# Optimization experiments

Measured on AMD Instinct MI355X. Metric: run time of the kernel, lower is better.

The kernel has to match this reference:

```python
import jax, jax.numpy as jnp
import numpy as np

N = 50000   # nodes
E = 800000  # edges (avg degree 16)
G = 256     # graphs in batch
IN = 64; H = 128; K = 8; C = 10; L = 3
TAU = 1.0


def _bn(x, g, b, eps=1e-5):
    # BatchNorm1d training-mode forward: batch stats over the row dim.
    m = x.mean(0)
    v = x.var(0)
    return (x - m) * jax.lax.rsqrt(v + eps) * g + b


def _ln(x, g, b, eps=1e-5):
    m = x.mean(-1, keepdims=True)
    v = x.var(-1, keepdims=True)
    return (x - m) * jax.lax.rsqrt(v + eps) * g + b


def setup_inputs() -> dict:
    key = jax.random.key(0)
    ks = jax.random.split(key, 16)
    p = lambda k, shape: jax.random.normal(k, shape, jnp.float32) * 0.05
    u = jax.random.uniform(ks[2], (N, K), minval=1e-10, maxval=1.0)
    return {
        "x": jax.random.normal(ks[0], (N, IN), jnp.float32),
        "edge_index": jax.random.randint(ks[1], (2, E), 0, N, dtype=jnp.int32),
        "batch": (jnp.arange(N, dtype=jnp.int32) * G) // N,  # sorted, all graphs present
        "gumbel": -jnp.log(-jnp.log(u)),  # fixed Gumbel(0,1) noise
        "inp_w": p(ks[3], (IN, H)), "inp_b": jnp.zeros(H),
        "elin_w": p(ks[4], (L, 1, H)), "elin_b": jnp.zeros((L, H)),
        "mlp1_w": p(ks[5], (L, H, H)), "mlp1_b": jnp.zeros((L, H)),
        "mlpbn_g": jnp.ones((L, H)), "mlpbn_b": jnp.zeros((L, H)),
        "mlp2_w": p(ks[6], (L, H, H)), "mlp2_b": jnp.zeros((L, H)),
        "bn_g": jnp.ones((L, H)), "bn_b": jnp.zeros((L, H)),
        "bh1_w": p(ks[7], (H, H // 2)), "bh1_b": jnp.zeros(H // 2),
        "bh2_w": p(ks[8], (H // 2, K)), "bh2_b": jnp.zeros(K),
        "bm_w": p(ks[9], (H, H)), "bm_b": jnp.zeros(H),
        "ln_g": jnp.ones(H), "ln_b": jnp.zeros(H),
        "clf1_w": p(ks[10], (2 * H, H)), "clf1_b": jnp.zeros(H),
        "clfbn_g": jnp.ones(H), "clfbn_b": jnp.zeros(H),
        "clf2_w": p(ks[11], (H, C)), "clf2_b": jnp.zeros(C),
    }


def reference(x, edge_index, batch, gumbel, inp_w, inp_b, elin_w, elin_b,
              mlp1_w, mlp1_b, mlpbn_g, mlpbn_b, mlp2_w, mlp2_b, bn_g, bn_b,
              bh1_w, bh1_b, bh2_w, bh2_b, bm_w, bm_b, ln_g, ln_b,
              clf1_w, clf1_b, clfbn_g, clfbn_b, clf2_w, clf2_b):
    src, dst = edge_index[0], edge_index[1]
    h = x @ inp_w + inp_b  # [N,H]
    for l in range(L):  # GINEConv stack (eps=0, dummy edge attr = ones[E,1])
        e_emb = elin_w[l][0] + elin_b[l]          # ones @ W + b -> single [H] vector
        msg = jax.nn.relu(h[src] + e_emb)          # gather + add, [E,H]
        aggr = jax.ops.segment_sum(msg, dst, num_segments=N)  # scatter-add
        z = h + aggr                               # (1+eps)*x + aggr, eps=0
        z = jax.nn.relu(_bn(z @ mlp1_w[l] + mlp1_b[l], mlpbn_g[l], mlpbn_b[l]))
        z = z @ mlp2_w[l] + mlp2_b[l]
        h = jax.nn.relu(_bn(z, bn_g[l], bn_b[l]))
    # blob assignment via gumbel-softmax (soft)
    logits = jax.nn.relu(h @ bh1_w + bh1_b) @ bh2_w + bh2_b  # [N,K]
    assign = jax.nn.softmax((logits + gumbel) / TAU, axis=-1)
    counts = jax.ops.segment_sum(jnp.ones((N,), h.dtype), batch, num_segments=G)
    gmean = jax.ops.segment_sum(h, batch, num_segments=G) / counts[:, None]  # [G,H]
    # per-graph weighted blob pooling, vectorized over graphs via segment_sum
    num = jax.ops.segment_sum(assign[:, :, None] * h[:, None, :], batch, num_segments=G)  # [G,K,H]
    den = jax.ops.segment_sum(assign, batch, num_segments=G)  # [G,K]
    blobs = num / (den[:, :, None] + 1e-8)
    blobs = _ln(jax.nn.relu(blobs @ bm_w + bm_b), ln_g, ln_b)
    blob_emb = blobs.max(axis=1)  # [G,H]
    z = jnp.concatenate([gmean, blob_emb], axis=-1)  # [G,2H]
    z = jax.nn.relu(_bn(z @ clf1_w + clf1_b, clfbn_g, clfbn_b))
    return z @ clf2_w + clf2_b  # [G,C]
```

## Files before the change

### kernel.cpp

```cpp
#include <hip/hip_runtime.h>
#include <hip/hip_bf16.h>


#define HH 128
typedef unsigned short u16;
typedef unsigned int u32;
typedef __attribute__((ext_vector_type(8))) short bf16x8;
typedef __attribute__((ext_vector_type(4))) float f32x4;

__device__ __forceinline__ void atomAddF(float* p, float v) { unsafeAtomicAdd(p, v); }

__device__ __forceinline__ u16 f2bf(float f) {
    u32 u = __float_as_uint(f);
    u += 0x7fffu + ((u >> 16) & 1u);
    return (u16)(u >> 16);
}
__device__ __forceinline__ float bf2f_lo(u32 u) { return __uint_as_float(u << 16); }
__device__ __forceinline__ float bf2f_hi(u32 u) { return __uint_as_float(u & 0xffff0000u); }
__device__ __forceinline__ void split2(float v, u16& hi, u16& lo) {
    u16 h_ = f2bf(v);
    float hf = __uint_as_float(((u32)h_) << 16);
    hi = h_;
    lo = f2bf(v - hf);
}
__device__ __forceinline__ u32 swz(u32 row, u32 kByte, u32 strideB) {
    return (row * strideB + kByte) ^ ((row & 7u) << 4);
}

#define WTOT (8192 + 6 * 16384)

__global__ void k_prep(const float* __restrict__ inp_w, const float* __restrict__ m1,
                       const float* __restrict__ m2, u16* __restrict__ Whi,
                       u16* __restrict__ Wlo) {
    int b = blockIdx.x;
    int t = threadIdx.x;
    if (b == 0) {
        for (int idx = t; idx < 128 * 64; idx += 256) {
            int c = idx >> 6, k = idx & 63;
            u16 hi, lo;
            split2(inp_w[k * 128 + c], hi, lo);
            Whi[idx] = hi; Wlo[idx] = lo;
        }
    } else {
        const float* W = (b <= 3) ? m1 + (size_t)(b - 1) * 16384
                                  : m2 + (size_t)(b - 4) * 16384;
        u16* dh = Whi + 8192 + (size_t)(b - 1) * 16384;
        u16* dl = Wlo + 8192 + (size_t)(b - 1) * 16384;
        for (int idx = t; idx < 16384; idx += 256) {
            int c = idx >> 7, k = idx & 127;
            u16 hi, lo;
            split2(W[k * 128 + c], hi, lo);
            dh[idx] = hi; dl[idx] = lo;
        }
    }
}

__global__ void k_hist(const int* __restrict__ ei, int* __restrict__ deg, int E) {
    int i4 = blockIdx.x * 256 + threadIdx.x;
    int e0 = i4 * 4;
    if (e0 + 3 < E) {
        int4 d = *(const int4*)(ei + E + e0);
        atomicAdd(&deg[d.x], 1);
        atomicAdd(&deg[d.y], 1);
        atomicAdd(&deg[d.z], 1);
        atomicAdd(&deg[d.w], 1);
    } else {
        for (int e = e0; e < E; e++) atomicAdd(&deg[ei[E + e]], 1);
    }
}

__global__ void k_bsum(const int* __restrict__ deg, int* __restrict__ bsum, int N) {
    int t = threadIdx.x;
    int i = blockIdx.x * 256 + t;
    int v = (i < N) ? deg[i] : 0;
    for (int o = 32; o; o >>= 1) v += __shfl_down(v, o);
    __shared__ int ws_[4];
    if ((t & 63) == 0) ws_[t >> 6] = v;
    __syncthreads();
    if (t == 0) bsum[blockIdx.x] = ws_[0] + ws_[1] + ws_[2] + ws_[3];
}

__global__ void k_scan1(const int* __restrict__ bsum, int* __restrict__ boff,
                        int* __restrict__ rowptrN, int nch) {
    int t = threadIdx.x;
    int v = (t < nch) ? bsum[t] : 0;
    int l = t & 63, w = t >> 6;
    int sv = v;
    for (int o = 1; o < 64; o <<= 1) { int u = __shfl_up(sv, o); if (l >= o) sv += u; }
    __shared__ int wsum[4];
    if (l == 63) wsum[w] = sv;
    __syncthreads();
    int add = 0;
    for (int j = 0; j < w; j++) add += wsum[j];
    if (t < nch) boff[t] = sv - v + add;
    if (t == nch - 1) *rowptrN = sv + add;
}

__global__ void k_scan2(const int* __restrict__ deg, const int* __restrict__ boff,
                        int* __restrict__ rowptr, int* __restrict__ cursor, int N) {
    int b = blockIdx.x, t = threadIdx.x, i = b * 256 + t;
    int v = (i < N) ? deg[i] : 0;
    int l = t & 63, w = t >> 6;
    int sv = v;
    for (int o = 1; o < 64; o <<= 1) { int u = __shfl_up(sv, o); if (l >= o) sv += u; }
    __shared__ int wsum[4];
    if (l == 63) wsum[w] = sv;
    __syncthreads();
    int add = boff[b];
    for (int j = 0; j < w; j++) add += wsum[j];
    if (i < N) { int e = sv - v + add; rowptr[i] = e; cursor[i] = e; }
}

__global__ void k_fill(const int* __restrict__ ei, int* __restrict__ cursor,
                       int* __restrict__ col, int E) {
    int i4 = blockIdx.x * 256 + threadIdx.x;
    int e0 = i4 * 4;
    if (e0 + 3 < E) {
        int4 s = *(const int4*)(ei + e0);
        int4 d = *(const int4*)(ei + E + e0);
        int p0 = atomicAdd(&cursor[d.x], 1);
        int p1 = atomicAdd(&cursor[d.y], 1);
        int p2 = atomicAdd(&cursor[d.z], 1);
        int p3 = atomicAdd(&cursor[d.w], 1);
        col[p0] = s.x;
        col[p1] = s.y;
        col[p2] = s.z;
        col[p3] = s.w;
    } else {
        for (int e = e0; e < E; e++) {
            int pos = atomicAdd(&cursor[ei[E + e]], 1);
            col[pos] = ei[e];
        }
    }
}

template <int KD, int MODE, bool STATS, bool FOUT, bool BOUT>
__global__ __launch_bounds__(512) void k_mgemm(
    const float* __restrict__ inf, const u16* __restrict__ inhi,
    const u16* __restrict__ inlo, const u16* __restrict__ Whi,
    const u16* __restrict__ Wlo, const float* __restrict__ bias,
    const float* __restrict__ statsIn, const float* __restrict__ gamma,
    const float* __restrict__ beta, float invN,
    float* __restrict__ out, u16* __restrict__ outb,
    float* __restrict__ statsOut, int Nrows, int ntiles) {
    __shared__ u16 s_Bhi[128 * KD];
    __shared__ u16 s_Blo[128 * KD];
    __shared__ float s_red[2][8][128];
    __shared__ float s_sc[128], s_sh[128];
    const int t = threadIdx.x;
    constexpr u32 STR = KD * 2;
    constexpr int KCB = KD / 8;
    constexpr int NB = (128 * KCB) / 512;
    constexpr int NF = KD / 32;

#pragma unroll
    for (int i = 0; i < NB; i++) {
        int idx = i * 512 + t;
        int c = idx / KCB, kc = idx % KCB;
        u32 off = swz(c, kc * 16, STR);
        *(uint4*)((char*)s_Bhi + off) = *(const uint4*)(Whi + (size_t)c * KD + kc * 8);
        *(uint4*)((char*)s_Blo + off) = *(const uint4*)(Wlo + (size_t)c * KD + kc * 8);
    }
    if (MODE == 1 && t < 128) {
        float m = statsIn[t] * invN;
        float var = statsIn[128 + t] * invN - m * m;
        float s = gamma[t] * rsqrtf(var + 1e-5f);
        s_sc[t] = s;
        s_sh[t] = beta[t] - m * s;
    }
    __syncthreads();

    const int l = t & 63, w = t >> 6;
    const int c0 = l & 15;
    const int ksub = (l >> 4) * 8;
    const u32 kOffB = (u32)(l >> 4) * 16u;

    for (int tile = blockIdx.x; tile < ntiles; tile += gridDim.x) {
        const int row = tile * 128 + w * 16 + c0;
        const bool rv = row < Nrows;

        bf16x8 ah[NF], al[NF];
        if (MODE == 2) {
#pragma unroll
            for (int kk = 0; kk < NF; kk++) {
                int k0 = kk * 32 + ksub;
                if (rv) {
                    ah[kk] = *(const bf16x8*)(inhi + (size_t)row * KD + k0);
                    al[kk] = *(const bf16x8*)(inlo + (size_t)row * KD + k0);
                } else {
                    uint4 z = {0, 0, 0, 0};
                    ah[kk] = *(bf16x8*)&z;
                    al[kk] = *(bf16x8*)&z;
                }
            }
        } else {
#pragma unroll
            for (int kk = 0; kk < NF; kk++) {
                int k0 = kk * 32 + ksub;
                float4 v0 = {0.f, 0.f, 0.f, 0.f}, v1 = {0.f, 0.f, 0.f, 0.f};
                if (rv) {
                    v0 = *(const float4*)(inf + (size_t)row * KD + k0);
                    v1 = *(const float4*)(inf + (size_t)row * KD + k0 + 4);
                }
                float vv[8] = {v0.x, v0.y, v0.z, v0.w, v1.x, v1.y, v1.z, v1.w};
                uint4 uh, ul;
                u32* ph = (u32*)&uh;
                u32* pl = (u32*)&ul;
#pragma unroll
                for (int p = 0; p < 4; p++) {
                    float a0 = vv[2 * p], a1 = vv[2 * p + 1];
                    if (MODE == 1) {
                        a0 = fmaxf(a0 * s_sc[k0 + 2 * p] + s_sh[k0 + 2 * p], 0.f);
                        a1 = fmaxf(a1 * s_sc[k0 + 2 * p + 1] + s_sh[k0 + 2 * p + 1], 0.f);
                    }
                    u16 h0, l0, h1, l1;
                    split2(a0, h0, l0);
                    split2(a1, h1, l1);
                    ph[p] = (u32)h0 | ((u32)h1 << 16);
                    pl[p] = (u32)l0 | ((u32)l1 << 16);
                }
                ah[kk] = *(bf16x8*)&uh;
                al[kk] = *(bf16x8*)&ul;
            }
        }

        f32x4 acc[8];
#pragma unroll
        for (int n = 0; n < 8; n++) acc[n] = (f32x4){0.f, 0.f, 0.f, 0.f};
#pragma unroll
        for (int kk = 0; kk < NF; kk++) {
            u32 kb = kk * 64 + kOffB;
#pragma unroll
            for (int n = 0; n < 8; n++) {
                u32 ob = swz(n * 16 + c0, kb, STR);
                bf16x8 bh = *(const bf16x8*)((char*)s_Bhi + ob);
                bf16x8 bl = *(const bf16x8*)((char*)s_Blo + ob);
                acc[n] = __builtin_amdgcn_mfma_f32_16x16x32_bf16(ah[kk], bh, acc[n], 0, 0, 0);
                acc[n] = __builtin_amdgcn_mfma_f32_16x16x32_bf16(al[kk], bh, acc[n], 0, 0, 0);
                acc[n] = __builtin_amdgcn_mfma_f32_16x16x32_bf16(ah[kk], bl, acc[n], 0, 0, 0);
            }
        }

        const int rbase = tile * 128 + w * 16 + ((l >> 4) << 2);
#pragma unroll
        for (int n = 0; n < 8; n++) {
            const int colc = n * 16 + c0;
            const float bv = bias[colc];
            float s = 0.f, q = 0.f;
#pragma unroll
            for (int j = 0; j < 4; j++) {
                int gr = rbase + j;
                if (gr < Nrows) {
                    float v = acc[n][j] + bv;
                    if (FOUT) out[(size_t)gr * HH + colc] = v;
                    if (BOUT) outb[(size_t)gr * HH + colc] = f2bf(v);
                    s += v;
                    q += v * v;
                }
            }
            if (STATS) {
                s += __shfl_xor(s, 16); s += __shfl_xor(s, 32);
                q += __shfl_xor(q, 16); q += __shfl_xor(q, 32);
                if (l < 16) {
                    s_red[0][w][n * 16 + l] = s;
                    s_red[1][w][n * 16 + l] = q;
                }
            }
        }
        if (STATS) {
            __syncthreads();
            if (t < 128) {
                float S = 0.f, Q = 0.f;
#pragma unroll
                for (int ww = 0; ww < 8; ww++) { S += s_red[0][ww][t]; Q += s_red[1][ww][t]; }
                atomAddF(&statsOut[t], S);
                atomAddF(&statsOut[HH + t], Q);
            }
            __syncthreads();
        }
    }
}

__global__ __launch_bounds__(256) void k_gather(
    const u16* __restrict__ hb,
    const int* __restrict__ rowptr, const int* __restrict__ col,
    const float* __restrict__ ew, const float* __restrict__ eb,
    u16* __restrict__ zhi, u16* __restrict__ zlo, int N) {
    __shared__ float2 s_part[2][64];
    const int wv = threadIdx.x >> 6;
    const int lane = threadIdx.x & 63;
    const int node = blockIdx.x * 2 + (wv >> 1);
    const int hf = wv & 1;
    const int c2 = lane * 2;
    float2 acc = {0.f, 0.f};
    const bool valid = node < N;
    float2 ee = {0.f, 0.f};
    if (valid) {
        ee.x = ew[c2] + eb[c2];
        ee.y = ew[c2 + 1] + eb[c2 + 1];
        const int s = rowptr[node], eend = rowptr[node + 1];
        int e = s + hf;
        for (; e + 14 < eend; e += 16) {
            int s0 = col[e], s1 = col[e + 2], s2 = col[e + 4], s3 = col[e + 6];
            int s4 = col[e + 8], s5 = col[e + 10], s6 = col[e + 12], s7 = col[e + 14];
            u32 u0 = *(const u32*)(hb + (size_t)s0 * HH + c2);
            u32 u1 = *(const u32*)(hb + (size_t)s1 * HH + c2);
            u32 u2 = *(const u32*)(hb + (size_t)s2 * HH + c2);
            u32 u3 = *(const u32*)(hb + (size_t)s3 * HH + c2);
            u32 u4 = *(const u32*)(hb + (size_t)s4 * HH + c2);
            u32 u5 = *(const u32*)(hb + (size_t)s5 * HH + c2);
            u32 u6 = *(const u32*)(hb + (size_t)s6 * HH + c2);
            u32 u7 = *(const u32*)(hb + (size_t)s7 * HH + c2);
            acc.x += fmaxf(bf2f_lo(u0) + ee.x, 0.f) + fmaxf(bf2f_lo(u1) + ee.x, 0.f) +
                     fmaxf(bf2f_lo(u2) + ee.x, 0.f) + fmaxf(bf2f_lo(u3) + ee.x, 0.f) +
                     fmaxf(bf2f_lo(u4) + ee.x, 0.f) + fmaxf(bf2f_lo(u5) + ee.x, 0.f) +
                     fmaxf(bf2f_lo(u6) + ee.x, 0.f) + fmaxf(bf2f_lo(u7) + ee.x, 0.f);
            acc.y += fmaxf(bf2f_hi(u0) + ee.y, 0.f) + fmaxf(bf2f_hi(u1) + ee.y, 0.f) +
                     fmaxf(bf2f_hi(u2) + ee.y, 0.f) + fmaxf(bf2f_hi(u3) + ee.y, 0.f) +
                     fmaxf(bf2f_hi(u4) + ee.y, 0.f) + fmaxf(bf2f_hi(u5) + ee.y, 0.f) +
                     fmaxf(bf2f_hi(u6) + ee.y, 0.f) + fmaxf(bf2f_hi(u7) + ee.y, 0.f);
        }
        for (; e + 6 < eend; e += 8) {
            int s0 = col[e], s1 = col[e + 2], s2 = col[e + 4], s3 = col[e + 6];
            u32 u0 = *(const u32*)(hb + (size_t)s0 * HH + c2);
            u32 u1 = *(const u32*)(hb + (size_t)s1 * HH + c2);
            u32 u2 = *(const u32*)(hb + (size_t)s2 * HH + c2);
            u32 u3 = *(const u32*)(hb + (size_t)s3 * HH + c2);
            acc.x += fmaxf(bf2f_lo(u0) + ee.x, 0.f) + fmaxf(bf2f_lo(u1) + ee.x, 0.f) +
                     fmaxf(bf2f_lo(u2) + ee.x, 0.f) + fmaxf(bf2f_lo(u3) + ee.x, 0.f);
            acc.y += fmaxf(bf2f_hi(u0) + ee.y, 0.f) + fmaxf(bf2f_hi(u1) + ee.y, 0.f) +
                     fmaxf(bf2f_hi(u2) + ee.y, 0.f) + fmaxf(bf2f_hi(u3) + ee.y, 0.f);
        }
        for (; e < eend; e += 2) {
            u32 u0 = *(const u32*)(hb + (size_t)col[e] * HH + c2);
            acc.x += fmaxf(bf2f_lo(u0) + ee.x, 0.f);
            acc.y += fmaxf(bf2f_hi(u0) + ee.y, 0.f);
        }
    }
    if (hf) s_part[wv >> 1][lane] = acc;
    __syncthreads();
    if (!hf && valid) {
        float2 p = s_part[wv >> 1][lane];
        u32 un = *(const u32*)(hb + (size_t)node * HH + c2);
        float zx = bf2f_lo(un) + acc.x + p.x;
        float zy = bf2f_hi(un) + acc.y + p.y;
        u16 h0, h1, l0, l1;
        split2(zx, h0, l0);
        split2(zy, h1, l1);
        *(u32*)(zhi + (size_t)node * HH + c2) = (u32)h0 | ((u32)h1 << 16);
        *(u32*)(zlo + (size_t)node * HH + c2) = (u32)l0 | ((u32)l1 << 16);
    }
}

template <bool WF>
__global__ void k_bnrelu(const float* __restrict__ t, const float* __restrict__ stats,
                         const float* __restrict__ g, const float* __restrict__ b,
                         float invN, float* __restrict__ h, u16* __restrict__ hb,
                         int total4) {
    int i = blockIdx.x * 256 + threadIdx.x;
    if (i >= total4) return;
    int c4 = (i & 31) << 2;
    float sc[4], sh[4];
#pragma unroll
    for (int j = 0; j < 4; j++) {
        float m = stats[c4 + j] * invN;
        float var = stats[128 + c4 + j] * invN - m * m;
        float s = g[c4 + j] * rsqrtf(var + 1e-5f);
        sc[j] = s;
        sh[j] = b[c4 + j] - m * s;
    }
    float4 v = *(const float4*)(t + (size_t)i * 4);
    float4 o;
    o.x = fmaxf(v.x * sc[0] + sh[0], 0.f);
    o.y = fmaxf(v.y * sc[1] + sh[1], 0.f);
    o.z = fmaxf(v.z * sc[2] + sh[2], 0.f);
    o.w = fmaxf(v.w * sc[3] + sh[3], 0.f);
    if (WF) *(float4*)(h + (size_t)i * 4) = o;
    uint2 p = {(u32)f2bf(o.x) | ((u32)f2bf(o.y) << 16),
               (u32)f2bf(o.z) | ((u32)f2bf(o.w) << 16)};
    *(uint2*)(hb + (size_t)i * 4) = p;
}

__global__ __launch_bounds__(256) void k_assign(
    const float* __restrict__ h, const float* __restrict__ gum,
    const float* __restrict__ w1, const float* __restrict__ b1,
    const float* __restrict__ w2, const float* __restrict__ b2,
    float* __restrict__ assign, int N) {
    __shared__ float s_w1[128 * 64];
    __shared__ float s_w2[64 * 8];
    __shared__ float s_h[32][128];
    __shared__ float s_hid[32][64];
    const int t = threadIdx.x;
    const int n0 = blockIdx.x * 32;
    for (int i = t; i < 128 * 64; i += 256) s_w1[i] = w1[i];
    for (int i = t; i < 512; i += 256) s_w2[i] = w2[i];
    for (int i = t; i < 32 * 32; i += 256) {
        int r = i >> 5, c4 = (i & 31) << 2;
        int gn = n0 + r;
        float4 v = {0.f, 0.f, 0.f, 0.f};
        if (gn < N) v = *(const float4*)(h + (size_t)gn * HH + c4);
        *(float4*)(&s_h[r][c4]) = v;
    }
    __syncthreads();
    for (int o = t; o < 32 * 64; o += 256) {
        int nn = o >> 6, j = o & 63;
        float acc = b1[j];
        for (int k = 0; k < 128; k++) acc = fmaf(s_h[nn][k], s_w1[k * 64 + j], acc);
        s_hid[nn][j] = fmaxf(acc, 0.f);
    }
    __syncthreads();
    int nn = t >> 3, kk = t & 7;
    int gn = n0 + nn;
    float a = b2[kk];
    for (int j = 0; j < 64; j++) a = fmaf(s_hid[nn][j], s_w2[j * 8 + kk], a);
    if (gn < N) a += gum[(size_t)gn * 8 + kk];
    float m = a;
    m = fmaxf(m, __shfl_xor(m, 1));
    m = fmaxf(m, __shfl_xor(m, 2));
    m = fmaxf(m, __shfl_xor(m, 4));
    float e = expf(a - m);
    float s = e;
    s += __shfl_xor(s, 1); s += __shfl_xor(s, 2); s += __shfl_xor(s, 4);
    if (gn < N) assign[(size_t)gn * 8 + kk] = e / s;
}

__device__ __forceinline__ int lowerb(const int* __restrict__ arr, int n, int val) {
    int lo = 0, hi = n;
    while (lo < hi) {
        int mid = (lo + hi) >> 1;
        if (arr[mid] < val) lo = mid + 1;
        else hi = mid;
    }
    return lo;
}

__global__ __launch_bounds__(1024) void k_pool(
    const float* __restrict__ h, const float* __restrict__ assign,
    const int* __restrict__ batch, float* __restrict__ gmean,
    float* __restrict__ num, float* __restrict__ den, int N) {
    __shared__ float4 s_num[4][8][32];
    __shared__ float4 s_gm[4][32];
    __shared__ float s_den[4][8];
    const int g = blockIdx.x;
    const int t = threadIdx.x;
    const int ns = t >> 8;
    const int k = (t >> 5) & 7;
    const int lane = t & 31;
    const int c4 = lane << 2;
    const int start = lowerb(batch, N, g);
    const int end = lowerb(batch, N, g + 1);
    float4 an = {0.f, 0.f, 0.f, 0.f};
    float4 gm = {0.f, 0.f, 0.f, 0.f};
    float ad = 0.f;
    for (int n = start + ns; n < end; n += 4) {
        float a = assign[(size_t)n * 8 + k];
        const float4 hv = *(const float4*)(h + (size_t)n * HH + c4);
        an.x = fmaf(a, hv.x, an.x);
        an.y = fmaf(a, hv.y, an.y);
        an.z = fmaf(a, hv.z, an.z);
        an.w = fmaf(a, hv.w, an.w);
        if (k == 0) { gm.x += hv.x; gm.y += hv.y; gm.z += hv.z; gm.w += hv.w; }
        ad += a;
    }
    s_num[ns][k][lane] = an;
    if (k == 0) s_gm[ns][lane] = gm;
    if (lane == 0) s_den[ns][k] = ad;
    __syncthreads();
    if (t < 256) {
        float4 a0 = s_num[0][k][lane], a1 = s_num[1][k][lane];
        float4 a2 = s_num[2][k][lane], a3 = s_num[3][k][lane];
        float4 o = {a0.x + a1.x + a2.x + a3.x, a0.y + a1.y + a2.y + a3.y,
                    a0.z + a1.z + a2.z + a3.z, a0.w + a1.w + a2.w + a3.w};
        *(float4*)(num + ((size_t)g * 8 + k) * HH + c4) = o;
        if (t < 32) {
            float4 g0 = s_gm[0][lane], g1 = s_gm[1][lane];
            float4 g2 = s_gm[2][lane], g3 = s_gm[3][lane];
            int cnt = end - start;
            float inv = 1.f / (float)(cnt > 0 ? cnt : 1);
            float4 om = {(g0.x + g1.x + g2.x + g3.x) * inv,
                         (g0.y + g1.y + g2.y + g3.y) * inv,
                         (g0.z + g1.z + g2.z + g3.z) * inv,
                         (g0.w + g1.w + g2.w + g3.w) * inv};
            *(float4*)(gmean + (size_t)g * HH + c4) = om;
        }
        if (t < 8) den[(size_t)g * 8 + t] =
            s_den[0][t] + s_den[1][t] + s_den[2][t] + s_den[3][t];
    }
}

__global__ void k_blob(const float* __restrict__ num, const float* __restrict__ den,
                       const float* __restrict__ w, const float* __restrict__ b,
                       const float* __restrict__ lg, const float* __restrict__ lb,
                       float* __restrict__ blobs) {
    const int gk = blockIdx.x;
    const int c = threadIdx.x;
    __shared__ float srow[128];
    __shared__ float red[4];
    float d = den[gk] + 1e-8f;
    srow[c] = num[(size_t)gk * HH + c] / d;
    __syncthreads();
    float acc = b[c];
    for (int j = 0; j < 128; j++) acc = fmaf(srow[j], w[j * HH + c], acc);
    float y = fmaxf(acc, 0.f);
    float s = y, q = y * y;
    for (int off = 32; off > 0; off >>= 1) {
        s += __shfl_down(s, off);
        q += __shfl_down(q, off);
    }
    if ((c & 63) == 0) { red[(c >> 6) * 2] = s; red[(c >> 6) * 2 + 1] = q; }
    __syncthreads();
    float S = red[0] + red[2], Q = red[1] + red[3];
    float m = S * (1.f / 128.f);
    float var = Q * (1.f / 128.f) - m * m;
    blobs[(size_t)gk * HH + c] = (y - m) * rsqrtf(var + 1e-5f) * lg[c] + lb[c];
}

__global__ void k_clf1(const float* __restrict__ gmean, const float* __restrict__ blobs,
                       const float* __restrict__ w, const float* __restrict__ bias,
                       float* __restrict__ t4, float* __restrict__ stats) {
    int g = blockIdx.x;
    int c = threadIdx.x;
    __shared__ float s[256];
    float m = blobs[((size_t)g * 8) * HH + c];
#pragma unroll
    for (int k = 1; k < 8; k++) m = fmaxf(m, blobs[((size_t)g * 8 + k) * HH + c]);
    s[c] = gmean[(size_t)g * HH + c];
    s[128 + c] = m;
    __syncthreads();
    float acc = bias[c];
    for (int j = 0; j < 256; j++) acc = fmaf(s[j], w[j * HH + c], acc);
    t4[(size_t)g * HH + c] = acc;
    atomAddF(&stats[c], acc);
    atomAddF(&stats[HH + c], acc * acc);
}

__global__ void k_clf2(const float* __restrict__ t4, const float* __restrict__ stats,
                       const float* __restrict__ g_, const float* __restrict__ b_,
                       float invG, const float* __restrict__ w,
                       const float* __restrict__ bias, float* __restrict__ out) {
    int g = blockIdx.x;
    int t = threadIdx.x;
    __shared__ float s[128];
    float m = stats[t] * invG;
    float var = stats[128 + t] * invG - m * m;
    float sc = g_[t] * rsqrtf(var + 1e-5f);
    float sh = b_[t] - m * sc;
    s[t] = fmaxf(t4[(size_t)g * HH + t] * sc + sh, 0.f);
    __syncthreads();
    if (t < 10) {
        float acc = bias[t];
        for (int j = 0; j < 128; j++) acc = fmaf(s[j], w[j * 10 + t], acc);
        out[(size_t)g * 10 + t] = acc;
    }
}

extern "C" void kernel_launch(void* const* d_in, const int* in_sizes, int n_in,
                              void* d_out, int out_size, void* d_ws, size_t ws_size,
                              hipStream_t stream) {
    const float* x      = (const float*)d_in[0];
    const int*   ei     = (const int*)d_in[1];
    const int*   batch  = (const int*)d_in[2];
    const float* gumbel = (const float*)d_in[3];
    const float* inp_w  = (const float*)d_in[4];
    const float* inp_b  = (const float*)d_in[5];
    const float* elin_w = (const float*)d_in[6];
    const float* elin_b = (const float*)d_in[7];
    const float* mlp1_w = (const float*)d_in[8];
    const float* mlp1_b = (const float*)d_in[9];
    const float* mlpbn_g = (const float*)d_in[10];
    const float* mlpbn_b = (const float*)d_in[11];
    const float* mlp2_w = (const float*)d_in[12];
    const float* mlp2_b = (const float*)d_in[13];
    const float* bn_g   = (const float*)d_in[14];
    const float* bn_b   = (const float*)d_in[15];
    const float* bh1_w  = (const float*)d_in[16];
    const float* bh1_b  = (const float*)d_in[17];
    const float* bh2_w  = (const float*)d_in[18];
    const float* bh2_b  = (const float*)d_in[19];
    const float* bm_w   = (const float*)d_in[20];
    const float* bm_b   = (const float*)d_in[21];
    const float* ln_g   = (const float*)d_in[22];
    const float* ln_b   = (const float*)d_in[23];
    const float* clf1_w = (const float*)d_in[24];
    const float* clf1_b = (const float*)d_in[25];
    const float* clfbn_g = (const float*)d_in[26];
    const float* clfbn_b = (const float*)d_in[27];
    const float* clf2_w = (const float*)d_in[28];
    const float* clf2_b = (const float*)d_in[29];
    float* out = (float*)d_out;

    const int N = in_sizes[0] / 64;
    const int E = in_sizes[1] / 2;
    const int G = out_size / 10;

    float* ws = (float*)d_ws;
    float* h      = ws;
    float* zbuf   = h + (size_t)N * HH;
    float* t1     = zbuf + (size_t)N * HH;
    float* assign = t1 + (size_t)N * HH;
    float* gmean  = assign + (size_t)N * 8;
    float* num    = gmean + (size_t)G * HH;
    float* den    = num + (size_t)G * 8 * HH;
    float* blobs  = den + (size_t)G * 8;
    float* t4     = blobs + (size_t)G * 8 * HH;
    float* statsA = t4 + (size_t)G * HH;
    u16* Whi = (u16*)(statsA + 7 * 256);
    u16* Wlo = Whi + WTOT;
    int* rowptr = (int*)(Wlo + WTOT);
    int* cursor = rowptr + (N + 1);
    int* colidx = cursor + N;
    int* bsum   = colidx + E;
    int* boff   = bsum + 256;
    u16* hb  = (u16*)t1;
    u16* zhi = (u16*)zbuf;
    u16* zlo = zhi + (size_t)N * HH;
    float* t2 = zbuf;

    const dim3 B256(256), B128(128), B512(512), B1024(1024);
    const int ntiles = (N + 127) / 128;
    const int gg = ntiles < 512 ? ntiles : 512;
    const int nch = (N + 255) / 256;
    const int e4 = (E + 4 * 256 - 1) / (4 * 256);
    const float invN = 1.f / (float)N;
    const float invG = 1.f / (float)G;

    k_prep<<<7, B256, 0, stream>>>(inp_w, mlp1_w, mlp2_w, Whi, Wlo);
    hipMemsetAsync(cursor, 0, (size_t)N * sizeof(int), stream);
    hipMemsetAsync(statsA, 0, 7 * 256 * sizeof(float), stream);
    k_hist<<<e4, B256, 0, stream>>>(ei, cursor, E);
    k_bsum<<<nch, B256, 0, stream>>>(cursor, bsum, N);
    k_scan1<<<1, B256, 0, stream>>>(bsum, boff, rowptr + N, nch);
    k_scan2<<<nch, B256, 0, stream>>>(cursor, boff, rowptr, cursor, N);
    k_fill<<<e4, B256, 0, stream>>>(ei, cursor, colidx, E);

    k_mgemm<64, 0, false, false, true><<<gg, B512, 0, stream>>>(
        x, nullptr, nullptr, Whi, Wlo, inp_b, nullptr, nullptr, nullptr, 0.f,
        nullptr, hb, nullptr, N, ntiles);

    for (int l = 0; l < 3; l++) {
        float* sa = statsA + (size_t)(2 * l) * 256;
        float* sb = statsA + (size_t)(2 * l + 1) * 256;
        k_gather<<<(N + 1) / 2, B256, 0, stream>>>(hb, rowptr, colidx,
                                                   elin_w + l * HH, elin_b + l * HH,
                                                   zhi, zlo, N);
        k_mgemm<128, 2, true, true, false><<<gg, B512, 0, stream>>>(
            nullptr, zhi, zlo, Whi + 8192 + (size_t)l * 16384,
            Wlo + 8192 + (size_t)l * 16384, mlp1_b + l * HH,
            nullptr, nullptr, nullptr, 0.f, t1, nullptr, sa, N, ntiles);
        k_mgemm<128, 1, true, true, false><<<gg, B512, 0, stream>>>(
            t1, nullptr, nullptr, Whi + 8192 + (size_t)(3 + l) * 16384,
            Wlo + 8192 + (size_t)(3 + l) * 16384, mlp2_b + l * HH,
            sa, mlpbn_g + l * HH, mlpbn_b + l * HH, invN, t2, nullptr, sb, N, ntiles);
        if (l < 2)
            k_bnrelu<false><<<(N * 32 + 255) / 256, B256, 0, stream>>>(
                t2, sb, bn_g + l * HH, bn_b + l * HH, invN, nullptr, hb, N * 32);
        else
            k_bnrelu<true><<<(N * 32 + 255) / 256, B256, 0, stream>>>(
                t2, sb, bn_g + l * HH, bn_b + l * HH, invN, h, hb, N * 32);
    }

    k_assign<<<(N + 31) / 32, B256, 0, stream>>>(h, gumbel, bh1_w, bh1_b, bh2_w, bh2_b, assign, N);
    k_pool<<<G, B1024, 0, stream>>>(h, assign, batch, gmean, num, den, N);
    k_blob<<<G * 8, B128, 0, stream>>>(num, den, bm_w, bm_b, ln_g, ln_b, blobs);
    float* sc_ = statsA + 6 * 256;
    k_clf1<<<G, B128, 0, stream>>>(gmean, blobs, clf1_w, clf1_b, t4, sc_);
    k_clf2<<<G, B128, 0, stream>>>(t4, sc_, clfbn_g, clfbn_b, invG, clf2_w, clf2_b, out);
}
```

Baseline: 511.2 us.

## Fuse BN+ReLU into gather and merge pooling, blob and classifier tail kernels

The second MLP GEMM of layers 0-1 now writes raw pre-BN output as bf16. The next layer's gather applies the batch-norm scale/shift and ReLU on the fly, which removes two standalone BN+ReLU passes over the N×128 activations. The pooling, blob projection with LayerNorm, and first classifier layer are merged into one per-graph kernel that keeps intermediates in shared memory, cutting launches and global round-trips. The price is extra per-element math in the gather, the per-edge BN now runs on bf16-rounded pre-BN values, and the big tail block runs serial 128-long dot loops.

```diff
diff --git a/kernel.cpp b/kernel.cpp
--- a/kernel.cpp
+++ b/kernel.cpp
@@ -281,10 +281,13 @@
     }
 }
 
+template <int BN>
 __global__ __launch_bounds__(256) void k_gather(
-    const u16* __restrict__ hb,
+    const u16* __restrict__ act,
     const int* __restrict__ rowptr, const int* __restrict__ col,
     const float* __restrict__ ew, const float* __restrict__ eb,
+    const float* __restrict__ stats, const float* __restrict__ gamma,
+    const float* __restrict__ beta, float invN,
     u16* __restrict__ zhi, u16* __restrict__ zlo, int N) {
     __shared__ float2 s_part[2][64];
     const int wv = threadIdx.x >> 6;
@@ -295,6 +298,26 @@
     float2 acc = {0.f, 0.f};
     const bool valid = node < N;
     float2 ee = {0.f, 0.f};
+    float sc0 = 1.f, sh0 = 0.f, sc1 = 1.f, sh1 = 0.f;
+    if (BN) {
+        float m0 = stats[c2] * invN;
+        float v0 = stats[128 + c2] * invN - m0 * m0;
+        sc0 = gamma[c2] * rsqrtf(v0 + 1e-5f);
+        sh0 = beta[c2] - m0 * sc0;
+        float m1 = stats[c2 + 1] * invN;
+        float v1 = stats[128 + c2 + 1] * invN - m1 * m1;
+        sc1 = gamma[c2 + 1] * rsqrtf(v1 + 1e-5f);
+        sh1 = beta[c2 + 1] - m1 * sc1;
+    }
+    auto proc = [&](u32 u) {
+        float v0 = bf2f_lo(u), v1 = bf2f_hi(u);
+        if (BN) {
+            v0 = fmaxf(fmaf(v0, sc0, sh0), 0.f);
+            v1 = fmaxf(fmaf(v1, sc1, sh1), 0.f);
+        }
+        acc.x += fmaxf(v0 + ee.x, 0.f);
+        acc.y += fmaxf(v1 + ee.y, 0.f);
+    };
     if (valid) {
         ee.x = ew[c2] + eb[c2];
         ee.y = ew[c2 + 1] + eb[c2 + 1];
@@ -303,47 +326,42 @@
         for (; e + 14 < eend; e += 16) {
             int s0 = col[e], s1 = col[e + 2], s2 = col[e + 4], s3 = col[e + 6];
             int s4 = col[e + 8], s5 = col[e + 10], s6 = col[e + 12], s7 = col[e + 14];
-            u32 u0 = *(const u32*)(hb + (size_t)s0 * HH + c2);
-            u32 u1 = *(const u32*)(hb + (size_t)s1 * HH + c2);
-            u32 u2 = *(const u32*)(hb + (size_t)s2 * HH + c2);
-            u32 u3 = *(const u32*)(hb + (size_t)s3 * HH + c2);
-            u32 u4 = *(const u32*)(hb + (size_t)s4 * HH + c2);
-            u32 u5 = *(const u32*)(hb + (size_t)s5 * HH + c2);
-            u32 u6 = *(const u32*)(hb + (size_t)s6 * HH + c2);
-            u32 u7 = *(const u32*)(hb + (size_t)s7 * HH + c2);
-            acc.x += fmaxf(bf2f_lo(u0) + ee.x, 0.f) + fmaxf(bf2f_lo(u1) + ee.x, 0.f) +
-                     fmaxf(bf2f_lo(u2) + ee.x, 0.f) + fmaxf(bf2f_lo(u3) + ee.x, 0.f) +
-                     fmaxf(bf2f_lo(u4) + ee.x, 0.f) + fmaxf(bf2f_lo(u5) + ee.x, 0.f) +
-                     fmaxf(bf2f_lo(u6) + ee.x, 0.f) + fmaxf(bf2f_lo(u7) + ee.x, 0.f);
-            acc.y += fmaxf(bf2f_hi(u0) + ee.y, 0.f) + fmaxf(bf2f_hi(u1) + ee.y, 0.f) +
-                     fmaxf(bf2f_hi(u2) + ee.y, 0.f) + fmaxf(bf2f_hi(u3) + ee.y, 0.f) +
-                     fmaxf(bf2f_hi(u4) + ee.y, 0.f) + fmaxf(bf2f_hi(u5) + ee.y, 0.f) +
-                     fmaxf(bf2f_hi(u6) + ee.y, 0.f) + fmaxf(bf2f_hi(u7) + ee.y, 0.f);
+            u32 u0 = *(const u32*)(act + (size_t)s0 * HH + c2);
+            u32 u1 = *(const u32*)(act + (size_t)s1 * HH + c2);
+            u32 u2 = *(const u32*)(act + (size_t)s2 * HH + c2);
+            u32 u3 = *(const u32*)(act + (size_t)s3 * HH + c2);
+            u32 u4 = *(const u32*)(act + (size_t)s4 * HH + c2);
+            u32 u5 = *(const u32*)(act + (size_t)s5 * HH + c2);
+            u32 u6 = *(const u32*)(act + (size_t)s6 * HH + c2);
+            u32 u7 = *(const u32*)(act + (size_t)s7 * HH + c2);
+            proc(u0); proc(u1); proc(u2); proc(u3);
+            proc(u4); proc(u5); proc(u6); proc(u7);
         }
         for (; e + 6 < eend; e += 8) {
             int s0 = col[e], s1 = col[e + 2], s2 = col[e + 4], s3 = col[e + 6];
-            u32 u0 = *(const u32*)(hb + (size_t)s0 * HH + c2);
-            u32 u1 = *(const u32*)(hb + (size_t)s1 * HH + c2);
-            u32 u2 = *(const u32*)(hb + (size_t)s2 * HH + c2);
-            u32 u3 = *(const u32*)(hb + (size_t)s3 * HH + c2);
-            acc.x += fmaxf(bf2f_lo(u0) + ee.x, 0.f) + fmaxf(bf2f_lo(u1) + ee.x, 0.f) +
-                     fmaxf(bf2f_lo(u2) + ee.x, 0.f) + fmaxf(bf2f_lo(u3) + ee.x, 0.f);
-            acc.y += fmaxf(bf2f_hi(u0) + ee.y, 0.f) + fmaxf(bf2f_hi(u1) + ee.y, 0.f) +
-                     fmaxf(bf2f_hi(u2) + ee.y, 0.f) + fmaxf(bf2f_hi(u3) + ee.y, 0.f);
+            u32 u0 = *(const u32*)(act + (size_t)s0 * HH + c2);
+            u32 u1 = *(const u32*)(act + (size_t)s1 * HH + c2);
+            u32 u2 = *(const u32*)(act + (size_t)s2 * HH + c2);
+            u32 u3 = *(const u32*)(act + (size_t)s3 * HH + c2);
+            proc(u0); proc(u1); proc(u2); proc(u3);
         }
         for (; e < eend; e += 2) {
-            u32 u0 = *(const u32*)(hb + (size_t)col[e] * HH + c2);
-            acc.x += fmaxf(bf2f_lo(u0) + ee.x, 0.f);
-            acc.y += fmaxf(bf2f_hi(u0) + ee.y, 0.f);
+            u32 u0 = *(const u32*)(act + (size_t)col[e] * HH + c2);
+            proc(u0);
         }
     }
     if (hf) s_part[wv >> 1][lane] = acc;
     __syncthreads();
     if (!hf && valid) {
         float2 p = s_part[wv >> 1][lane];
-        u32 un = *(const u32*)(hb + (size_t)node * HH + c2);
-        float zx = bf2f_lo(un) + acc.x + p.x;
-        float zy = bf2f_hi(un) + acc.y + p.y;
+        u32 un = *(const u32*)(act + (size_t)node * HH + c2);
+        float s0 = bf2f_lo(un), s1 = bf2f_hi(un);
+        if (BN) {
+            s0 = fmaxf(fmaf(s0, sc0, sh0), 0.f);
+            s1 = fmaxf(fmaf(s1, sc1, sh1), 0.f);
+        }
+        float zx = s0 + acc.x + p.x;
+        float zy = s1 + acc.y + p.y;
         u16 h0, h1, l0, l1;
         split2(zx, h0, l0);
         split2(zy, h1, l1);
@@ -352,11 +370,9 @@
     }
 }
 
-template <bool WF>
 __global__ void k_bnrelu(const float* __restrict__ t, const float* __restrict__ stats,
                          const float* __restrict__ g, const float* __restrict__ b,
-                         float invN, float* __restrict__ h, u16* __restrict__ hb,
-                         int total4) {
+                         float invN, float* __restrict__ h, int total4) {
     int i = blockIdx.x * 256 + threadIdx.x;
     if (i >= total4) return;
     int c4 = (i & 31) << 2;
@@ -375,10 +391,7 @@
     o.y = fmaxf(v.y * sc[1] + sh[1], 0.f);
     o.z = fmaxf(v.z * sc[2] + sh[2], 0.f);
     o.w = fmaxf(v.w * sc[3] + sh[3], 0.f);
-    if (WF) *(float4*)(h + (size_t)i * 4) = o;
-    uint2 p = {(u32)f2bf(o.x) | ((u32)f2bf(o.y) << 16),
-               (u32)f2bf(o.z) | ((u32)f2bf(o.w) << 16)};
-    *(uint2*)(hb + (size_t)i * 4) = p;
+    *(float4*)(h + (size_t)i * 4) = o;
 }
 
 __global__ __launch_bounds__(256) void k_assign(
@@ -434,13 +447,21 @@
     return lo;
 }
 
-__global__ __launch_bounds__(1024) void k_pool(
+__global__ __launch_bounds__(1024) void k_tail(
     const float* __restrict__ h, const float* __restrict__ assign,
-    const int* __restrict__ batch, float* __restrict__ gmean,
-    float* __restrict__ num, float* __restrict__ den, int N) {
+    const int* __restrict__ batch, const float* __restrict__ bm_w,
+    const float* __restrict__ bm_b, const float* __restrict__ ln_g,
+    const float* __restrict__ ln_b, const float* __restrict__ clf1_w,
+    const float* __restrict__ clf1_b, float* __restrict__ t4,
+    float* __restrict__ stats, int N) {
     __shared__ float4 s_num[4][8][32];
     __shared__ float4 s_gm[4][32];
     __shared__ float s_den[4][8];
+    __shared__ float s_numf[8][128];
+    __shared__ float s_denf[8];
+    __shared__ float s_blob[8][128];
+    __shared__ float s_cat[256];
+    __shared__ float s_r[16][2];
     const int g = blockIdx.x;
     const int t = threadIdx.x;
     const int ns = t >> 8;
@@ -449,6 +470,7 @@
     const int c4 = lane << 2;
     const int start = lowerb(batch, N, g);
     const int end = lowerb(batch, N, g + 1);
+
     float4 an = {0.f, 0.f, 0.f, 0.f};
     float4 gm = {0.f, 0.f, 0.f, 0.f};
     float ad = 0.f;
@@ -469,69 +491,63 @@
     if (t < 256) {
         float4 a0 = s_num[0][k][lane], a1 = s_num[1][k][lane];
         float4 a2 = s_num[2][k][lane], a3 = s_num[3][k][lane];
-        float4 o = {a0.x + a1.x + a2.x + a3.x, a0.y + a1.y + a2.y + a3.y,
-                    a0.z + a1.z + a2.z + a3.z, a0.w + a1.w + a2.w + a3.w};
-        *(float4*)(num + ((size_t)g * 8 + k) * HH + c4) = o;
+        s_numf[k][c4 + 0] = a0.x + a1.x + a2.x + a3.x;
+        s_numf[k][c4 + 1] = a0.y + a1.y + a2.y + a3.y;
+        s_numf[k][c4 + 2] = a0.z + a1.z + a2.z + a3.z;
+        s_numf[k][c4 + 3] = a0.w + a1.w + a2.w + a3.w;
         if (t < 32) {
             float4 g0 = s_gm[0][lane], g1 = s_gm[1][lane];
             float4 g2 = s_gm[2][lane], g3 = s_gm[3][lane];
             int cnt = end - start;
             float inv = 1.f / (float)(cnt > 0 ? cnt : 1);
-            float4 om = {(g0.x + g1.x + g2.x + g3.x) * inv,
-                         (g0.y + g1.y + g2.y + g3.y) * inv,
-                         (g0.z + g1.z + g2.z + g3.z) * inv,
-                         (g0.w + g1.w + g2.w + g3.w) * inv};
-            *(float4*)(gmean + (size_t)g * HH + c4) = om;
-        }
-        if (t < 8) den[(size_t)g * 8 + t] =
-            s_den[0][t] + s_den[1][t] + s_den[2][t] + s_den[3][t];
-    }
-}
-
-__global__ void k_blob(const float* __restrict__ num, const float* __restrict__ den,
-                       const float* __restrict__ w, const float* __restrict__ b,
-                       const float* __restrict__ lg, const float* __restrict__ lb,
-                       float* __restrict__ blobs) {
-    const int gk = blockIdx.x;
-    const int c = threadIdx.x;
-    __shared__ float srow[128];
-    __shared__ float red[4];
-    float d = den[gk] + 1e-8f;
-    srow[c] = num[(size_t)gk * HH + c] / d;
-    __syncthreads();
-    float acc = b[c];
-    for (int j = 0; j < 128; j++) acc = fmaf(srow[j], w[j * HH + c], acc);
-    float y = fmaxf(acc, 0.f);
-    float s = y, q = y * y;
-    for (int off = 32; off > 0; off >>= 1) {
-        s += __shfl_down(s, off);
-        q += __shfl_down(q, off);
-    }
-    if ((c & 63) == 0) { red[(c >> 6) * 2] = s; red[(c >> 6) * 2 + 1] = q; }
-    __syncthreads();
-    float S = red[0] + red[2], Q = red[1] + red[3];
-    float m = S * (1.f / 128.f);
-    float var = Q * (1.f / 128.f) - m * m;
-    blobs[(size_t)gk * HH + c] = (y - m) * rsqrtf(var + 1e-5f) * lg[c] + lb[c];
-}
-
-__global__ void k_clf1(const float* __restrict__ gmean, const float* __restrict__ blobs,
-                       const float* __restrict__ w, const float* __restrict__ bias,
-                       float* __restrict__ t4, float* __restrict__ stats) {
-    int g = blockIdx.x;
-    int c = threadIdx.x;
-    __shared__ float s[256];
-    float m = blobs[((size_t)g * 8) * HH + c];
-#pragma unroll
-    for (int k = 1; k < 8; k++) m = fmaxf(m, blobs[((size_t)g * 8 + k) * HH + c]);
-    s[c] = gmean[(size_t)g * HH + c];
-    s[128 + c] = m;
-    __syncthreads();
-    float acc = bias[c];
-    for (int j = 0; j < 256; j++) acc = fmaf(s[j], w[j * HH + c], acc);
-    t4[(size_t)g * HH + c] = acc;
-    atomAddF(&stats[c], acc);
-    atomAddF(&stats[HH + c], acc * acc);
+            s_cat[c4 + 0] = (g0.x + g1.x + g2.x + g3.x) * inv;
+            s_cat[c4 + 1] = (g0.y + g1.y + g2.y + g3.y) * inv;
+            s_cat[c4 + 2] = (g0.z + g1.z + g2.z + g3.z) * inv;
+            s_cat[c4 + 3] = (g0.w + g1.w + g2.w + g3.w) * inv;
+        }
+        if (t < 8) s_denf[t] = s_den[0][t] + s_den[1][t] + s_den[2][t] + s_den[3][t];
+    }
+    __syncthreads();
+
+    {
+        const int kk = t >> 7;
+        const int c = t & 127;
+        const float d = 1.f / (s_denf[kk] + 1e-8f);
+        float acc = bm_b[c];
+        for (int j = 0; j < 128; j++)
+            acc = fmaf(s_numf[kk][j] * d, bm_w[j * HH + c], acc);
+        float y = fmaxf(acc, 0.f);
+        float s = y, q = y * y;
+        for (int off = 32; off > 0; off >>= 1) {
+            s += __shfl_down(s, off);
+            q += __shfl_down(q, off);
+        }
+        const int wv = t >> 6;
+        if ((t & 63) == 0) { s_r[wv][0] = s; s_r[wv][1] = q; }
+        __syncthreads();
+        float S = s_r[kk * 2][0] + s_r[kk * 2 + 1][0];
+        float Q = s_r[kk * 2][1] + s_r[kk * 2 + 1][1];
+        float m = S * (1.f / 128.f);
+        float var = Q * (1.f / 128.f) - m * m;
+        s_blob[kk][c] = (y - m) * rsqrtf(var + 1e-5f) * ln_g[c] + ln_b[c];
+    }
+    __syncthreads();
+
+    if (t < 128) {
+        float m = s_blob[0][t];
+#pragma unroll
+        for (int kk = 1; kk < 8; kk++) m = fmaxf(m, s_blob[kk][t]);
+        s_cat[128 + t] = m;
+    }
+    __syncthreads();
+
+    if (t < 128) {
+        float acc = clf1_b[t];
+        for (int j = 0; j < 256; j++) acc = fmaf(s_cat[j], clf1_w[j * HH + t], acc);
+        t4[(size_t)g * HH + t] = acc;
+        atomAddF(&stats[t], acc);
+        atomAddF(&stats[HH + t], acc * acc);
+    }
 }
 
 __global__ void k_clf2(const float* __restrict__ t4, const float* __restrict__ stats,
@@ -594,15 +610,11 @@
     const int G = out_size / 10;
 
     float* ws = (float*)d_ws;
-    float* h      = ws;
-    float* zbuf   = h + (size_t)N * HH;
-    float* t1     = zbuf + (size_t)N * HH;
-    float* assign = t1 + (size_t)N * HH;
-    float* gmean  = assign + (size_t)N * 8;
-    float* num    = gmean + (size_t)G * HH;
-    float* den    = num + (size_t)G * 8 * HH;
-    float* blobs  = den + (size_t)G * 8;
-    float* t4     = blobs + (size_t)G * 8 * HH;
+    float* A      = ws;
+    float* B      = A + (size_t)N * HH;
+    float* C      = B + (size_t)N * HH;
+    float* assign = C + (size_t)N * HH;
+    float* t4     = assign + (size_t)N * 8;
     float* statsA = t4 + (size_t)G * HH;
     u16* Whi = (u16*)(statsA + 7 * 256);
     u16* Wlo = Whi + WTOT;
@@ -611,10 +623,13 @@
     int* colidx = cursor + N;
     int* bsum   = colidx + E;
     int* boff   = bsum + 256;
-    u16* hb  = (u16*)t1;
-    u16* zhi = (u16*)zbuf;
-    u16* zlo = zhi + (size_t)N * HH;
-    float* t2 = zbuf;
+    u16* zhi  = (u16*)A;
+    u16* zlo  = zhi + (size_t)N * HH;
+    float* h  = A;
+    u16* t2b  = (u16*)B;
+    float* t2f = B;
+    u16* act0 = (u16*)C;
+    float* t1 = C;
 
     const dim3 B256(256), B128(128), B512(512), B1024(1024);
     const int ntiles = (N + 127) / 128;
@@ -635,34 +650,43 @@
 
     k_mgemm<64, 0, false, false, true><<<gg, B512, 0, stream>>>(
         x, nullptr, nullptr, Whi, Wlo, inp_b, nullptr, nullptr, nullptr, 0.f,
-        nullptr, hb, nullptr, N, ntiles);
+        nullptr, act0, nullptr, N, ntiles);
 
     for (int l = 0; l < 3; l++) {
         float* sa = statsA + (size_t)(2 * l) * 256;
-        float* sb = statsA + (size_t)(2 * l + 1) * 256;
-        k_gather<<<(N + 1) / 2, B256, 0, stream>>>(hb, rowptr, colidx,
-                                                   elin_w + l * HH, elin_b + l * HH,
-                                                   zhi, zlo, N);
+        float* sb = sa + 256;
+        if (l == 0)
+            k_gather<0><<<(N + 1) / 2, B256, 0, stream>>>(
+                act0, rowptr, colidx, elin_w, elin_b,
+                nullptr, nullptr, nullptr, 0.f, zhi, zlo, N);
+        else
+            k_gather<1><<<(N + 1) / 2, B256, 0, stream>>>(
+                t2b, rowptr, colidx, elin_w + l * HH, elin_b + l * HH,
+                statsA + (size_t)(2 * (l - 1) + 1) * 256,
+                bn_g + (l - 1) * HH, bn_b + (l - 1) * HH, invN, zhi, zlo, N);
         k_mgemm<128, 2, true, true, false><<<gg, B512, 0, stream>>>(
             nullptr, zhi, zlo, Whi + 8192 + (size_t)l * 16384,
             Wlo + 8192 + (size_t)l * 16384, mlp1_b + l * HH,
             nullptr, nullptr, nullptr, 0.f, t1, nullptr, sa, N, ntiles);
-        k_mgemm<128, 1, true, true, false><<<gg, B512, 0, stream>>>(
-            t1, nullptr, nullptr, Whi + 8192 + (size_t)(3 + l) * 16384,
-            Wlo + 8192 + (size_t)(3 + l) * 16384, mlp2_b + l * HH,
-            sa, mlpbn_g + l * HH, mlpbn_b + l * HH, invN, t2, nullptr, sb, N, ntiles);
         if (l < 2)
-            k_bnrelu<false><<<(N * 32 + 255) / 256, B256, 0, stream>>>(
-                t2, sb, bn_g + l * HH, bn_b + l * HH, invN, nullptr, hb, N * 32);
+            k_mgemm<128, 1, true, false, true><<<gg, B512, 0, stream>>>(
+                t1, nullptr, nullptr, Whi + 8192 + (size_t)(3 + l) * 16384,
+                Wlo + 8192 + (size_t)(3 + l) * 16384, mlp2_b + l * HH,
+                sa, mlpbn_g + l * HH, mlpbn_b + l * HH, invN,
+                nullptr, t2b, sb, N, ntiles);
         else
-            k_bnrelu<true><<<(N * 32 + 255) / 256, B256, 0, stream>>>(
-                t2, sb, bn_g + l * HH, bn_b + l * HH, invN, h, hb, N * 32);
-    }
+            k_mgemm<128, 1, true, true, false><<<gg, B512, 0, stream>>>(
+                t1, nullptr, nullptr, Whi + 8192 + (size_t)(3 + l) * 16384,
+                Wlo + 8192 + (size_t)(3 + l) * 16384, mlp2_b + l * HH,
+                sa, mlpbn_g + l * HH, mlpbn_b + l * HH, invN,
+                t2f, nullptr, sb, N, ntiles);
+    }
+    k_bnrelu<<<(N * 32 + 255) / 256, B256, 0, stream>>>(
+        t2f, statsA + 5 * 256, bn_g + 2 * HH, bn_b + 2 * HH, invN, h, N * 32);
 
     k_assign<<<(N + 31) / 32, B256, 0, stream>>>(h, gumbel, bh1_w, bh1_b, bh2_w, bh2_b, assign, N);
-    k_pool<<<G, B1024, 0, stream>>>(h, assign, batch, gmean, num, den, N);
-    k_blob<<<G * 8, B128, 0, stream>>>(num, den, bm_w, bm_b, ln_g, ln_b, blobs);
     float* sc_ = statsA + 6 * 256;
-    k_clf1<<<G, B128, 0, stream>>>(gmean, blobs, clf1_w, clf1_b, t4, sc_);
+    k_tail<<<G, B1024, 0, stream>>>(h, assign, batch, bm_w, bm_b, ln_g, ln_b,
+                                    clf1_w, clf1_b, t4, sc_, N);
     k_clf2<<<G, B128, 0, stream>>>(t4, sc_, clfbn_g, clfbn_b, invG, clf2_w, clf2_b, out);
 }
```

Result: no change. 501.4 us (-1.9%).
